# Optimization experiments

Hardware: AMD Instinct MI355X
Metric: run time of the kernel (lower is better)

The kernel has to match this reference:

```python
import jax, jax.numpy as jnp
import numpy as np

MARKER = 50251
BETA_FLOOR = 0.1
LOCAL_SCALE = 0.3
EPS = 1e-6
WINDOW = 256

B, T, D, H, K, V = 4, 1024, 1024, 16, 64, 64
HD = D // H  # SWA head dim


def setup_inputs() -> dict:
    key = jax.random.key(0)
    ks = jax.random.split(key, 16)
    p = lambda i, shape: jax.random.normal(ks[i], shape, jnp.float32) * 0.02
    return dict(
        x=jax.random.normal(ks[0], (B, T, D), jnp.float32),
        initial_state=jnp.zeros((B, H, K, V), jnp.float32),
        W_k=p(1, (D, H * K)),
        W_v=p(2, (D, H * V)),
        W_gdn_o=p(3, (H * V, D)),
        W_beta=p(4, (D, H)), b_beta=jnp.full((H,), -2.0, jnp.float32),
        W_g=p(5, (D, H)), b_g=jnp.full((H,), 2.0, jnp.float32),
        W_lq=p(6, (D, D)), W_lk=p(7, (D, D)), W_lv=p(8, (D, D)),
        W_swa_o=p(9, (D, D)),
        W_ret_o=p(10, (H * V, D)),
        W_gate=p(11, (D, H)), b_gate=jnp.ones((H,), jnp.float32),
        norm_w=jnp.ones((D,), jnp.float32),
        input_ids=jax.random.randint(ks[12], (B, T), 0, 50257, jnp.int32),
    )


def _delta_scan(k, v, beta, g, S0):
    # gated delta rule:  Sd = g_t * S_{t-1};  S_t = Sd + beta_t * k_t (v_t - k_t Sd);  o_t = k_t S_t
    # k:[B,Tm,H,K]  v:[B,Tm,H,V]  beta,g:[B,Tm,H]  S0:[B,H,K,V]
    def step(S, inp):
        kt, vt, bt, gt = inp  # [B,H,K],[B,H,V],[B,H],[B,H]
        Sd = gt[..., None, None] * S
        err = vt - jnp.einsum('bhk,bhkv->bhv', kt, Sd)
        Sn = Sd + bt[..., None, None] * (kt[..., None] * err[:, :, None, :])
        ot = jnp.einsum('bhk,bhkv->bhv', kt, Sn)
        return Sn, ot
    Sf, o = jax.lax.scan(step, S0, (k.transpose(1, 0, 2, 3), v.transpose(1, 0, 2, 3),
                                    beta.transpose(1, 0, 2), g.transpose(1, 0, 2)))
    return o.transpose(1, 0, 2, 3), Sf  # [B,Tm,H,V], [B,H,K,V]


def _forward(x, initial_state, W_k, W_v, W_gdn_o, W_beta, b_beta, W_g, b_g,
             W_lq, W_lk, W_lv, W_swa_o, W_ret_o, W_gate, b_gate, norm_w, input_ids):
    # RMSNorm
    rms = jnp.sqrt(jnp.mean(x * x, axis=-1, keepdims=True) + EPS)
    xn = x / rms * norm_w

    # shared L2-normalized keys and values
    k_shared = (xn @ W_k).reshape(B, T, H, K)
    k_shared = k_shared / jnp.maximum(jnp.linalg.norm(k_shared, axis=-1, keepdims=True), 1e-12)
    v_full = (xn @ W_v).reshape(B, T, H, V)

    # shifted-value GDN inputs (predict next token's value)
    k = k_shared[:, :-1]
    v = v_full[:, 1:]
    beta = jax.nn.sigmoid(xn[:, :-1] @ W_beta + b_beta)  # [B,T-1,H]
    g = jax.nn.sigmoid(xn[:, :-1] @ W_g + b_g)
    marker = (input_ids[:, :-1] == MARKER)[..., None]
    beta = beta * (BETA_FLOOR + (1.0 - BETA_FLOOR) * marker.astype(beta.dtype))

    o, Sf = _delta_scan(k, v, beta, g, initial_state)
    gdn_out = jnp.concatenate([jnp.zeros((B, 1, H, V), o.dtype), o], axis=1)
    gdn_out = gdn_out.reshape(B, T, H * V) @ W_gdn_o  # [B,T,D]

    # sliding-window attention (fallback masked-softmax path)
    q = (xn @ W_lq).reshape(B, T, H, HD).transpose(0, 2, 1, 3)
    kl = (xn @ W_lk).reshape(B, T, H, HD).transpose(0, 2, 1, 3)
    vl = (xn @ W_lv).reshape(B, T, H, HD).transpose(0, 2, 1, 3)
    scale = K ** (-0.5)
    i = jnp.arange(T)[:, None]
    j = jnp.arange(T)[None, :]
    allowed = (j <= i) & (j >= i - WINDOW)  # causal within window
    attn = jnp.einsum('bhqd,bhkd->bhqk', q, kl) * scale
    attn = jnp.where(allowed, attn, -jnp.inf)
    probs = jax.nn.softmax(attn, axis=-1)
    local = jnp.einsum('bhqk,bhkd->bhqd', probs, vl).transpose(0, 2, 1, 3).reshape(B, T, D)
    local_out = LOCAL_SCALE * (local @ W_swa_o)  # eval mode

    # retrieval from final state with shared keys as queries
    retrieved = jnp.einsum('bhkv,bthk->bthv', Sf, k_shared).reshape(B, T, H * V)
    retrieval_out = retrieved @ W_ret_o
    gate = jax.nn.sigmoid(xn @ W_gate + b_gate)  # [B,T,H]
    retrieval_out = jnp.mean(gate, axis=-1, keepdims=True) * retrieval_out

    return x + gdn_out + local_out + retrieval_out


def reference(x, initial_state, W_k, W_v, W_gdn_o, W_beta, b_beta, W_g, b_g,
              W_lq, W_lk, W_lv, W_swa_o, W_ret_o, W_gate, b_gate, norm_w, input_ids):
    return _forward(x, initial_state, W_k, W_v, W_gdn_o, W_beta, b_beta, W_g, b_g,
                    W_lq, W_lk, W_lv, W_swa_o, W_ret_o, W_gate, b_gate, norm_w, input_ids)
```

## Files before the change

kernel.cpp:

```cpp
#include <hip/hip_runtime.h>
#include <hip/hip_bf16.h>

#define BB 4
#define TT 1024
#define DD 1024
#define HH 16
#define KK 64
#define VV 64
#define WIN 256
#define MARKER_ID 50251
#define PSA 5120
#define PSB 3072
#define NPROJ 5248

typedef short bfrag8 __attribute__((ext_vector_type(8)));
typedef float f32x4 __attribute__((ext_vector_type(4)));

static __device__ __forceinline__ unsigned short f2bf(float f) {
  __hip_bfloat16 h = __float2bfloat16(f);
  union { __hip_bfloat16 h; unsigned short u; } cv;
  cv.h = h;
  return cv.u;
}
static __device__ __forceinline__ float bf2f(unsigned short u) {
  union { unsigned int i; float f; } c;
  c.i = ((unsigned int)u) << 16;
  return c.f;
}
static __device__ __forceinline__ void gld_lds16(const unsigned short* g,
                                                 unsigned short* l) {
  __builtin_amdgcn_global_load_lds(
      (const __attribute__((address_space(1))) void*)g,
      (__attribute__((address_space(3))) void*)l, 16, 0, 0);
}

__global__ __launch_bounds__(256) void rmsnorm_kernel(
    const float* __restrict__ x, const float* __restrict__ nw,
    unsigned short* __restrict__ xnb) {
  int row = blockIdx.x;
  int tid = threadIdx.x;
  const float4* xr = (const float4*)(x + (size_t)row * DD);
  float4 v = xr[tid];
  float ss = v.x * v.x + v.y * v.y + v.z * v.z + v.w * v.w;
#pragma unroll
  for (int off = 32; off; off >>= 1) ss += __shfl_xor(ss, off);
  __shared__ float red[4];
  int wid = tid >> 6;
  if ((tid & 63) == 0) red[wid] = ss;
  __syncthreads();
  float tot = red[0] + red[1] + red[2] + red[3];
  float inv = 1.0f / sqrtf(tot * (1.0f / DD) + 1e-6f);
  const float4* wr = (const float4*)nw;
  float4 wv = wr[tid];
  ushort4 o;
  o.x = f2bf(v.x * inv * wv.x);
  o.y = f2bf(v.y * inv * wv.y);
  o.z = f2bf(v.z * inv * wv.z);
  o.w = f2bf(v.w * inv * wv.w);
  *(ushort4*)&xnb[(size_t)row * DD + tid * 4] = o;
}

__global__ __launch_bounds__(256) void convert_wt_kernel(
    const float* W0, const float* W1, const float* W2, const float* W3,
    const float* W4, const float* W5, const float* W6, const float* W7,
    const float* Wb, const float* Wg, const float* Wgt,
    unsigned short* C5, unsigned short* C3) {
  int tid = threadIdx.x;
  if (blockIdx.z == 8) {
    if (blockIdx.x != 0) return;
    int k0 = blockIdx.y * 64;
    for (int e = tid; e < 3 * 16 * 64; e += 256) {
      int w = e >> 10;
      int h = (e >> 6) & 15;
      int kk = e & 63;
      const float* Ws = (w == 0) ? Wb : (w == 1) ? Wg : Wgt;
      C5[(size_t)(5120 + w * 16 + h) * 1024 + k0 + kk] =
          f2bf(Ws[(size_t)(k0 + kk) * 16 + h]);
    }
    for (int e = tid; e < 80 * 64; e += 256) {
      int r = e >> 6, kk = e & 63;
      C5[(size_t)(5168 + r) * 1024 + k0 + kk] = 0;
    }
    return;
  }
  const float* W;
  unsigned short* T;
  int stride;
  float scale = 1.f;
  switch (blockIdx.z) {
    case 0: W = W0; T = C5 + 0 * 1024 * 1024; stride = 1024; break;
    case 1: W = W1; T = C5 + 1 * 1024 * 1024; stride = 1024; break;
    case 2: W = W2; T = C5 + 2 * 1024 * 1024; stride = 1024; break;
    case 3: W = W3; T = C5 + 3 * 1024 * 1024; stride = 1024; break;
    case 4: W = W4; T = C5 + 4 * 1024 * 1024; stride = 1024; break;
    case 5: W = W5; T = C3 + 0; stride = PSB; break;
    case 6: W = W6; T = C3 + 1024; stride = PSB; scale = 0.3f; break;
    default: W = W7; T = C3 + 2048; stride = PSB; break;
  }
  __shared__ float Ts[64][68];
  int n0 = blockIdx.x * 64, k0 = blockIdx.y * 64;
#pragma unroll
  for (int p = 0; p < 4; ++p) {
    int e = p * 256 + tid;
    int k = e >> 4, nq = e & 15;
    float4 w = *(const float4*)&W[(size_t)(k0 + k) * 1024 + n0 + nq * 4];
    Ts[nq * 4 + 0][k] = w.x;
    Ts[nq * 4 + 1][k] = w.y;
    Ts[nq * 4 + 2][k] = w.z;
    Ts[nq * 4 + 3][k] = w.w;
  }
  __syncthreads();
#pragma unroll
  for (int p = 0; p < 4; ++p) {
    int e = p * 256 + tid;
    int n = e >> 4, kq = e & 15;
    float4 v = *(const float4*)&Ts[n][kq * 4];
    ushort4 u;
    u.x = f2bf(v.x * scale);
    u.y = f2bf(v.y * scale);
    u.z = f2bf(v.z * scale);
    u.w = f2bf(v.w * scale);
    *(ushort4*)&T[(size_t)(n0 + n) * stride + k0 + kq * 4] = u;
  }
}

__global__ __launch_bounds__(256) void gemm_out_kernel(
    const unsigned short* __restrict__ A, const unsigned short* __restrict__ BT,
    float* __restrict__ C, const float* __restrict__ addp, int M, int N,
    int K) {
  __shared__ unsigned short As[2][128][32];
  __shared__ unsigned short Bs[2][64][32];
  int flat = blockIdx.y * gridDim.x + blockIdx.x;
  int xcd = flat & 7, local = flat >> 3;
  int m0 = (xcd * 4 + (local & 3)) * 128;
  int n0 = (local >> 2) * 64;
  int tid = threadIdx.x;
  int wave = tid >> 6, lane = tid & 63;
  int wm = wave * 32;
  int r16 = lane & 15, quad = lane >> 4;
  int lrow = lane >> 2, lcol = (lane & 3) * 8;

  f32x4 acc[2][4];
#pragma unroll
  for (int i = 0; i < 2; ++i)
#pragma unroll
    for (int j = 0; j < 4; ++j) acc[i][j] = {0.f, 0.f, 0.f, 0.f};

  auto STAGE = [&](int buf, int kt) {
#pragma unroll
    for (int q = 0; q < 2; ++q) {
      int rb = (wave * 2 + q) * 16;
      gld_lds16(&A[(size_t)(m0 + rb + lrow) * K + kt + lcol], &As[buf][rb][0]);
    }
    {
      int rb = wave * 16;
      gld_lds16(&BT[(size_t)(n0 + rb + lrow) * K + kt + lcol], &Bs[buf][rb][0]);
    }
  };
  auto COMPUTE = [&](int buf) {
    bfrag8 af[2], bq[4];
#pragma unroll
    for (int i = 0; i < 2; ++i)
      af[i] = *(const bfrag8*)&As[buf][wm + i * 16 + r16][quad * 8];
#pragma unroll
    for (int j = 0; j < 4; ++j)
      bq[j] = *(const bfrag8*)&Bs[buf][j * 16 + r16][quad * 8];
#pragma unroll
    for (int i = 0; i < 2; ++i)
#pragma unroll
      for (int j = 0; j < 4; ++j)
        acc[i][j] = __builtin_amdgcn_mfma_f32_16x16x32_bf16(af[i], bq[j],
                                                            acc[i][j], 0, 0, 0);
  };

  STAGE(0, 0);
  STAGE(1, 32);
  asm volatile("s_waitcnt vmcnt(3)" ::: "memory");
  __builtin_amdgcn_s_barrier();
  __builtin_amdgcn_sched_barrier(0);

  int cur = 0;
  for (int kt = 64; kt < K; kt += 32) {
    COMPUTE(cur);
    __builtin_amdgcn_s_barrier();
    STAGE(cur, kt);
    asm volatile("s_waitcnt vmcnt(3)" ::: "memory");
    __builtin_amdgcn_s_barrier();
    __builtin_amdgcn_sched_barrier(0);
    cur ^= 1;
  }
  COMPUTE(cur);
  asm volatile("s_waitcnt vmcnt(0)" ::: "memory");
  __builtin_amdgcn_s_barrier();
  __builtin_amdgcn_sched_barrier(0);
  COMPUTE(cur ^ 1);

#pragma unroll
  for (int i = 0; i < 2; ++i) {
#pragma unroll
    for (int r = 0; r < 4; ++r) {
      int row = m0 + wm + i * 16 + quad * 4 + r;
#pragma unroll
      for (int j = 0; j < 4; ++j) {
        int col = n0 + j * 16 + r16;
        size_t idx = (size_t)row * N + col;
        C[idx] = addp[idx] + acc[i][j][r];
      }
    }
  }
}

__global__ __launch_bounds__(256, 4) void gemm_proj_kernel(
    const unsigned short* __restrict__ A, const unsigned short* __restrict__ BT,
    unsigned short* __restrict__ PALL, float* __restrict__ SPRJ) {
  const int K = 1024;
  __shared__ unsigned short As[2][128][32];
  __shared__ unsigned short Bs[2][128][32];
  int flat = blockIdx.y * gridDim.x + blockIdx.x;
  int xcd = flat & 7, local = flat >> 3;
  int mi = local & 3, ni = local >> 2;
  int m0 = (xcd * 4 + mi) * 128;
  int n0 = ni * 128;
  int tid = threadIdx.x;
  int wave = tid >> 6, lane = tid & 63;
  int wm = (wave & 1) * 64, wn = (wave >> 1) * 64;
  int r16 = lane & 15, quad = lane >> 4;
  int lrow = lane >> 2, lcol = (lane & 3) * 8;

  f32x4 acc[4][4];
#pragma unroll
  for (int i = 0; i < 4; ++i)
#pragma unroll
    for (int j = 0; j < 4; ++j) acc[i][j] = {0.f, 0.f, 0.f, 0.f};

#pragma unroll
  for (int q = 0; q < 2; ++q) {
    int rb = (wave * 2 + q) * 16;
    gld_lds16(&A[(size_t)(m0 + rb + lrow) * K + lcol], &As[0][rb][0]);
    gld_lds16(&BT[(size_t)(n0 + rb + lrow) * K + lcol], &Bs[0][rb][0]);
  }
  __syncthreads();

  int cur = 0;
  for (int kt = 32; kt < K; kt += 32) {
#pragma unroll
    for (int q = 0; q < 2; ++q) {
      int rb = (wave * 2 + q) * 16;
      gld_lds16(&A[(size_t)(m0 + rb + lrow) * K + kt + lcol],
                &As[cur ^ 1][rb][0]);
      gld_lds16(&BT[(size_t)(n0 + rb + lrow) * K + kt + lcol],
                &Bs[cur ^ 1][rb][0]);
    }
    bfrag8 af[4], bq[4];
#pragma unroll
    for (int i = 0; i < 4; ++i) {
      af[i] = *(const bfrag8*)&As[cur][wm + i * 16 + r16][quad * 8];
      bq[i] = *(const bfrag8*)&Bs[cur][wn + i * 16 + r16][quad * 8];
    }
#pragma unroll
    for (int i = 0; i < 4; ++i)
#pragma unroll
      for (int j = 0; j < 4; ++j)
        acc[i][j] = __builtin_amdgcn_mfma_f32_16x16x32_bf16(af[i], bq[j],
                                                            acc[i][j], 0, 0, 0);
    __syncthreads();
    cur ^= 1;
  }
  {
    bfrag8 af[4], bq[4];
#pragma unroll
    for (int i = 0; i < 4; ++i) {
      af[i] = *(const bfrag8*)&As[cur][wm + i * 16 + r16][quad * 8];
      bq[i] = *(const bfrag8*)&Bs[cur][wn + i * 16 + r16][quad * 8];
    }
#pragma unroll
    for (int i = 0; i < 4; ++i)
#pragma unroll
      for (int j = 0; j < 4; ++j)
        acc[i][j] = __builtin_amdgcn_mfma_f32_16x16x32_bf16(af[i], bq[j],
                                                            acc[i][j], 0, 0, 0);
  }
  bool gates = (n0 >= 5120);
#pragma unroll
  for (int i = 0; i < 4; ++i) {
#pragma unroll
    for (int r = 0; r < 4; ++r) {
      int row = m0 + wm + i * 16 + quad * 4 + r;
#pragma unroll
      for (int j = 0; j < 4; ++j) {
        int col = n0 + wn + j * 16 + r16;
        if (!gates)
          PALL[(size_t)row * PSA + col] = f2bf(acc[i][j][r]);
        else
          SPRJ[(size_t)row * 128 + col - 5120] = acc[i][j][r];
      }
    }
  }
}

__global__ __launch_bounds__(256) void gates_kernel(
    const float* __restrict__ SPRJ, const float* __restrict__ bb,
    const float* __restrict__ bg, const float* __restrict__ bgt,
    const int* __restrict__ ids, float* __restrict__ beta,
    float* __restrict__ g, float* __restrict__ mg) {
  int row = blockIdx.x * 4 + (threadIdx.x >> 6);
  int lane = threadIdx.x & 63;
  if (lane < 48) {
    int h = lane & 15;
    float v = SPRJ[(size_t)row * 128 + lane];
    float bias = (lane < 16) ? bb[h] : (lane < 32) ? bg[h] : bgt[h];
    float s = 1.f / (1.f + __expf(-(v + bias)));
    if (lane < 16) {
      float mk = (ids[row] == MARKER_ID) ? 1.f : 0.1f;
      beta[(size_t)row * 16 + h] = s * mk;
    } else if (lane < 32) {
      g[(size_t)row * 16 + h] = s;
    } else {
      float sum = s;
#pragma unroll
      for (int off = 1; off < 16; off <<= 1) sum += __shfl_xor(sum, off);
      if (lane == 32) mg[row] = sum * (1.f / 16.f);
    }
  }
}

__global__ __launch_bounds__(256) void knorm_kernel(
    unsigned short* __restrict__ pall) {
  int w = blockIdx.x * 4 + (threadIdx.x >> 6);
  int lane = threadIdx.x & 63;
  size_t addr = (size_t)(w >> 4) * PSA + (w & 15) * 64 + lane;
  float v = bf2f(pall[addr]);
  float ss = v * v;
#pragma unroll
  for (int off = 32; off; off >>= 1) ss += __shfl_xor(ss, off);
  float n = sqrtf(ss);
  n = fmaxf(n, 1e-12f);
  pall[addr] = f2bf(v / n);
}

__global__ __launch_bounds__(256) void attn_mfma_kernel(
    const unsigned short* __restrict__ PALL, unsigned short* __restrict__ ACAT) {
  __shared__ unsigned short Qs[64][72];
  __shared__ unsigned short Ks[64][72];
  __shared__ unsigned short Vt[64][72];
  __shared__ unsigned short Ps[64][72];
  int qb = blockIdx.x * 64;
  int bh = blockIdx.y;
  int h = bh & 15, b = bh >> 4;
  int tid = threadIdx.x, lane = tid & 63, wave = tid >> 6;
  int r16 = lane & 15, quad = lane >> 4;
  int m0w = wave * 16;
  const unsigned short* Qg = PALL + (size_t)b * TT * PSA + 2048 + h * 64;
  const unsigned short* Kg = Qg + 1024;
  const unsigned short* Vg = Qg + 2048;
  int sr = tid >> 2, sq = tid & 3;
  {
    *(uint4*)&Qs[sr][sq * 16] =
        *(const uint4*)&Qg[(size_t)(qb + sr) * PSA + sq * 16];
    *(uint4*)&Qs[sr][sq * 16 + 8] =
        *(const uint4*)&Qg[(size_t)(qb + sr) * PSA + sq * 16 + 8];
  }
  float m[4], l[4];
  f32x4 o[4];
#pragma unroll
  for (int r = 0; r < 4; ++r) {
    m[r] = -1e30f;
    l[r] = 0.f;
    o[r] = {0.f, 0.f, 0.f, 0.f};
  }
  int kt0 = qb - (int)WIN;
  if (kt0 < 0) kt0 = 0;

  for (int kt = kt0; kt <= qb; kt += 64) {
    __syncthreads();
    {
      *(uint4*)&Ks[sr][sq * 16] =
          *(const uint4*)&Kg[(size_t)(kt + sr) * PSA + sq * 16];
      *(uint4*)&Ks[sr][sq * 16 + 8] =
          *(const uint4*)&Kg[(size_t)(kt + sr) * PSA + sq * 16 + 8];
      union { uint4 u4[2]; unsigned short s[16]; } vv;
      vv.u4[0] = *(const uint4*)&Vg[(size_t)(kt + sr) * PSA + sq * 16];
      vv.u4[1] = *(const uint4*)&Vg[(size_t)(kt + sr) * PSA + sq * 16 + 8];
#pragma unroll
      for (int i = 0; i < 16; ++i) Vt[sq * 16 + i][sr] = vv.s[i];
    }
    __syncthreads();
    bfrag8 af0 = *(const bfrag8*)&Qs[m0w + r16][quad * 8];
    bfrag8 af1 = *(const bfrag8*)&Qs[m0w + r16][quad * 8 + 32];
    f32x4 s[4];
#pragma unroll
    for (int j = 0; j < 4; ++j) s[j] = {0.f, 0.f, 0.f, 0.f};
#pragma unroll
    for (int j = 0; j < 4; ++j) {
      bfrag8 b0 = *(const bfrag8*)&Ks[j * 16 + r16][quad * 8];
      bfrag8 b1 = *(const bfrag8*)&Ks[j * 16 + r16][quad * 8 + 32];
      s[j] = __builtin_amdgcn_mfma_f32_16x16x32_bf16(af0, b0, s[j], 0, 0, 0);
      s[j] = __builtin_amdgcn_mfma_f32_16x16x32_bf16(af1, b1, s[j], 0, 0, 0);
    }
    bool oldest = (kt == qb - (int)WIN);
    bool newest = (kt == qb);
#pragma unroll
    for (int r = 0; r < 4; ++r) {
      int il = m0w + quad * 4 + r;
      float sv[4];
#pragma unroll
      for (int j = 0; j < 4; ++j) {
        int jl = j * 16 + r16;
        float v = s[j][r] * 0.125f;
        if (oldest && jl < il) v = -1e30f;
        if (newest && jl > il) v = -1e30f;
        sv[j] = v;
      }
      float mx = fmaxf(fmaxf(sv[0], sv[1]), fmaxf(sv[2], sv[3]));
#pragma unroll
      for (int off = 1; off < 16; off <<= 1) mx = fmaxf(mx, __shfl_xor(mx, off));
      float mn = fmaxf(m[r], mx);
      float al = __expf(m[r] - mn);
      m[r] = mn;
      float rs = 0.f;
#pragma unroll
      for (int j = 0; j < 4; ++j) {
        float p = __expf(sv[j] - mn);
        rs += p;
        Ps[il][j * 16 + r16] = f2bf(p);
      }
#pragma unroll
      for (int off = 1; off < 16; off <<= 1) rs += __shfl_xor(rs, off);
      l[r] = l[r] * al + rs;
#pragma unroll
      for (int j = 0; j < 4; ++j) o[j][r] *= al;
    }
    bfrag8 pa0 = *(const bfrag8*)&Ps[m0w + r16][quad * 8];
    bfrag8 pa1 = *(const bfrag8*)&Ps[m0w + r16][quad * 8 + 32];
#pragma unroll
    for (int j = 0; j < 4; ++j) {
      bfrag8 v0 = *(const bfrag8*)&Vt[j * 16 + r16][quad * 8];
      bfrag8 v1 = *(const bfrag8*)&Vt[j * 16 + r16][quad * 8 + 32];
      o[j] = __builtin_amdgcn_mfma_f32_16x16x32_bf16(pa0, v0, o[j], 0, 0, 0);
      o[j] = __builtin_amdgcn_mfma_f32_16x16x32_bf16(pa1, v1, o[j], 0, 0, 0);
    }
  }
#pragma unroll
  for (int r = 0; r < 4; ++r) {
    int row = m0w + quad * 4 + r;
    float inv = 1.f / l[r];
#pragma unroll
    for (int j = 0; j < 4; ++j) {
      ACAT[((size_t)(b * TT + qb + row)) * PSB + 1024 + h * 64 + j * 16 + r16] =
          f2bf(o[j][r] * inv);
    }
  }
}

__global__ __launch_bounds__(256) void scan_phaseA(
    const unsigned short* __restrict__ PALL, const float* __restrict__ beta,
    const float* __restrict__ g, unsigned short* __restrict__ UFg,
    unsigned short* __restrict__ Zg, unsigned short* __restrict__ Pg,
    unsigned short* __restrict__ Qg, float* __restrict__ Ag) {
  __shared__ unsigned short Kc[64][72];
  __shared__ unsigned short KTb[64][72];
  __shared__ float Vc[64][68];
  __shared__ float Msv[64][68];
  __shared__ unsigned short UFT[64][72];
  __shared__ unsigned short ZTl[64][72];
  __shared__ float aArr[64], iaArr[64], bArr[64], baArr[64], sKT[64];
  __shared__ float aCs;

  int c = blockIdx.x, bh = blockIdx.y;
  int b = bh >> 4, h = bh & 15;
  int tc = c * 64;
  int tid = threadIdx.x, lane = tid & 63, wave = tid >> 6;
  int r16 = lane & 15, quad = lane >> 4;
  int m0w = wave * 16;
  size_t bhc = (size_t)bh * 16 + c;

  const unsigned short* kbase = PALL + ((size_t)b * TT) * PSA + h * 64;
  const unsigned short* vbase = kbase + 1024;
  const float* bbase = beta + ((size_t)b * TT) * HH + h;
  const float* gbase = g + ((size_t)b * TT) * HH + h;

  if (tid < 64) {
    int ts = tc + tid;
    bool pad = (ts > 1022);
    float gv = pad ? 1.f : gbase[(size_t)ts * HH];
    float bv = pad ? 0.f : bbase[(size_t)ts * HH];
    float p = gv;
#pragma unroll
    for (int o = 1; o < 64; o <<= 1) {
      float t = __shfl_up(p, o);
      if (lane >= o) p *= t;
    }
    aArr[tid] = p;
    iaArr[tid] = 1.f / p;
    bArr[tid] = bv;
    baArr[tid] = bv * p;
    float aC = __shfl(p, 63);
    sKT[tid] = aC / p;
    if (tid == 0) aCs = aC;
    Ag[bhc * 64 + tid] = p;
  }
  __syncthreads();
  {
    int r = tid >> 2, q = tid & 3;
    int ts = tc + r;
    float skt = sKT[r];
    union { uint4 u4[2]; unsigned short s[16]; } kv;
    kv.u4[0] = *(const uint4*)&kbase[(size_t)ts * PSA + q * 16];
    kv.u4[1] = *(const uint4*)&kbase[(size_t)ts * PSA + q * 16 + 8];
    *(uint4*)&Kc[r][q * 16] = kv.u4[0];
    *(uint4*)&Kc[r][q * 16 + 8] = kv.u4[1];
#pragma unroll
    for (int i = 0; i < 16; ++i)
      KTb[q * 16 + i][r] = f2bf(bf2f(kv.s[i]) * skt);
    if (ts <= 1022) {
      union { uint4 u4[2]; unsigned short s[16]; } vv;
      vv.u4[0] = *(const uint4*)&vbase[(size_t)(ts + 1) * PSA + q * 16];
      vv.u4[1] = *(const uint4*)&vbase[(size_t)(ts + 1) * PSA + q * 16 + 8];
#pragma unroll
      for (int i = 0; i < 16; ++i) Vc[r][q * 16 + i] = bf2f(vv.s[i]);
    } else {
#pragma unroll
      for (int i = 0; i < 16; ++i) Vc[r][q * 16 + i] = 0.f;
    }
  }
  __syncthreads();
  {
    bfrag8 af0 = *(const bfrag8*)&Kc[m0w + r16][quad * 8];
    bfrag8 af1 = *(const bfrag8*)&Kc[m0w + r16][quad * 8 + 32];
    f32x4 acc1[4];
#pragma unroll
    for (int j = 0; j < 4; ++j) acc1[j] = {0.f, 0.f, 0.f, 0.f};
#pragma unroll
    for (int j = 0; j < 4; ++j) {
      bfrag8 k0 = *(const bfrag8*)&Kc[j * 16 + r16][quad * 8];
      bfrag8 k1 = *(const bfrag8*)&Kc[j * 16 + r16][quad * 8 + 32];
      acc1[j] = __builtin_amdgcn_mfma_f32_16x16x32_bf16(af0, k0, acc1[j], 0, 0, 0);
      acc1[j] = __builtin_amdgcn_mfma_f32_16x16x32_bf16(af1, k1, acc1[j], 0, 0, 0);
    }
#pragma unroll
    for (int j = 0; j < 4; ++j) {
#pragma unroll
      for (int r = 0; r < 4; ++r) {
        int row = m0w + quad * 4 + r;
        int col = j * 16 + r16;
        Msv[row][col] =
            (col < row) ? bArr[row] * aArr[row] * iaArr[col] * acc1[j][r] : 0.f;
      }
    }
  }
  __syncthreads();
  if (wave < 2) {
    float u[64];
    if (wave == 0) {
#pragma unroll
      for (int t = 0; t < 64; ++t) u[t] = bArr[t] * Vc[t][lane];
    } else {
#pragma unroll
      for (int t = 0; t < 64; ++t) u[t] = baArr[t] * bf2f(Kc[t][lane]);
    }
#pragma unroll
    for (int t = 1; t < 64; ++t) {
      float a0 = 0.f, a1 = 0.f, a2 = 0.f, a3 = 0.f;
#pragma unroll
      for (int s4 = 0; s4 * 4 < t; ++s4) {
        float4 mr = *(const float4*)&Msv[t][s4 * 4];
        a0 = fmaf(mr.x, u[s4 * 4 + 0], a0);
        a1 = fmaf(mr.y, u[s4 * 4 + 1], a1);
        a2 = fmaf(mr.z, u[s4 * 4 + 2], a2);
        a3 = fmaf(mr.w, u[s4 * 4 + 3], a3);
      }
      u[t] -= (a0 + a1) + (a2 + a3);
    }
    unsigned short* Tls = (wave == 0) ? &UFT[lane][0] : &ZTl[lane][0];
#pragma unroll
    for (int t2 = 0; t2 < 32; ++t2) {
      unsigned int pk = (unsigned int)f2bf(u[2 * t2]) |
                        ((unsigned int)f2bf(u[2 * t2 + 1]) << 16);
      *(unsigned int*)&Tls[2 * t2] = pk;
    }
    unsigned short* Gn = (wave == 0) ? UFg : Zg;
#pragma unroll
    for (int t = 0; t < 64; ++t) {
      Gn[(bhc * 64 + t) * 64 + lane] = f2bf(u[t]);
    }
  }
  __syncthreads();
  {
    bfrag8 af0 = *(const bfrag8*)&KTb[m0w + r16][quad * 8];
    bfrag8 af1 = *(const bfrag8*)&KTb[m0w + r16][quad * 8 + 32];
    f32x4 accp[4], accq[4];
#pragma unroll
    for (int j = 0; j < 4; ++j) {
      accp[j] = {0.f, 0.f, 0.f, 0.f};
      accq[j] = {0.f, 0.f, 0.f, 0.f};
    }
#pragma unroll
    for (int j = 0; j < 4; ++j) {
      bfrag8 z0 = *(const bfrag8*)&ZTl[j * 16 + r16][quad * 8];
      bfrag8 z1 = *(const bfrag8*)&ZTl[j * 16 + r16][quad * 8 + 32];
      accp[j] = __builtin_amdgcn_mfma_f32_16x16x32_bf16(af0, z0, accp[j], 0, 0, 0);
      accp[j] = __builtin_amdgcn_mfma_f32_16x16x32_bf16(af1, z1, accp[j], 0, 0, 0);
      bfrag8 u0 = *(const bfrag8*)&UFT[j * 16 + r16][quad * 8];
      bfrag8 u1 = *(const bfrag8*)&UFT[j * 16 + r16][quad * 8 + 32];
      accq[j] = __builtin_amdgcn_mfma_f32_16x16x32_bf16(af0, u0, accq[j], 0, 0, 0);
      accq[j] = __builtin_amdgcn_mfma_f32_16x16x32_bf16(af1, u1, accq[j], 0, 0, 0);
    }
    float aC = aCs;
#pragma unroll
    for (int j = 0; j < 4; ++j) {
#pragma unroll
      for (int r = 0; r < 4; ++r) {
        int row = m0w + quad * 4 + r;
        int col = j * 16 + r16;
        float pv = ((row == col) ? aC : 0.f) - accp[j][r];
        Pg[bhc * 4096 + (size_t)row * 64 + col] = f2bf(pv);
        Qg[bhc * 4096 + (size_t)row * 64 + col] = f2bf(accq[j][r]);
      }
    }
  }
}

__global__ __launch_bounds__(256) void scan_phaseB(
    const float* __restrict__ S0, const unsigned short* __restrict__ Pg,
    const unsigned short* __restrict__ Qg, unsigned short* __restrict__ SinTg,
    float* __restrict__ Sf, unsigned short* __restrict__ ACAT) {
  __shared__ unsigned short STb[64][72];
  __shared__ unsigned short Pl[64][72];
  int bh = blockIdx.x;
  int b = bh >> 4, h = bh & 15;
  int tid = threadIdx.x, lane = tid & 63, wave = tid >> 6;
  int r16 = lane & 15, quad = lane >> 4;
  int m0w = wave * 16;
  int rr = tid >> 2, qq = tid & 3;
  {
    const float* s0p = S0 + (size_t)bh * 4096;
#pragma unroll
    for (int i = 0; i < 4; ++i) {
      float4 sv = *(const float4*)&s0p[rr * 64 + qq * 16 + i * 4];
      STb[qq * 16 + i * 4 + 0][rr] = f2bf(sv.x);
      STb[qq * 16 + i * 4 + 1][rr] = f2bf(sv.y);
      STb[qq * 16 + i * 4 + 2][rr] = f2bf(sv.z);
      STb[qq * 16 + i * 4 + 3][rr] = f2bf(sv.w);
    }
    if (tid < 64) ACAT[((size_t)b * TT) * PSB + h * 64 + tid] = 0;
  }
  for (int c = 0; c < 16; ++c) {
    size_t bhc = (size_t)bh * 16 + c;
    __syncthreads();
    {
      uint4 s0v = *(const uint4*)&STb[rr][qq * 16];
      uint4 s1v = *(const uint4*)&STb[rr][qq * 16 + 8];
      *(uint4*)&SinTg[bhc * 4096 + (size_t)rr * 64 + qq * 16] = s0v;
      *(uint4*)&SinTg[bhc * 4096 + (size_t)rr * 64 + qq * 16 + 8] = s1v;
      uint4 p0 = *(const uint4*)&Pg[bhc * 4096 + (size_t)rr * 64 + qq * 16];
      uint4 p1 = *(const uint4*)&Pg[bhc * 4096 + (size_t)rr * 64 + qq * 16 + 8];
      *(uint4*)&Pl[rr][qq * 16] = p0;
      *(uint4*)&Pl[rr][qq * 16 + 8] = p1;
    }
    __syncthreads();
    f32x4 acc[4];
#pragma unroll
    for (int j = 0; j < 4; ++j) acc[j] = {0.f, 0.f, 0.f, 0.f};
    {
      bfrag8 af0 = *(const bfrag8*)&Pl[m0w + r16][quad * 8];
      bfrag8 af1 = *(const bfrag8*)&Pl[m0w + r16][quad * 8 + 32];
#pragma unroll
      for (int j = 0; j < 4; ++j) {
        bfrag8 s0v = *(const bfrag8*)&STb[j * 16 + r16][quad * 8];
        bfrag8 s1v = *(const bfrag8*)&STb[j * 16 + r16][quad * 8 + 32];
        acc[j] = __builtin_amdgcn_mfma_f32_16x16x32_bf16(af0, s0v, acc[j], 0, 0, 0);
        acc[j] = __builtin_amdgcn_mfma_f32_16x16x32_bf16(af1, s1v, acc[j], 0, 0, 0);
      }
    }
    float snew[4][4];
#pragma unroll
    for (int j = 0; j < 4; ++j) {
#pragma unroll
      for (int r = 0; r < 4; ++r) {
        int row = m0w + quad * 4 + r;
        int col = j * 16 + r16;
        snew[j][r] = acc[j][r] + bf2f(Qg[bhc * 4096 + (size_t)row * 64 + col]);
      }
    }
    __syncthreads();
#pragma unroll
    for (int j = 0; j < 4; ++j) {
#pragma unroll
      for (int r = 0; r < 4; ++r) {
        int row = m0w + quad * 4 + r;
        int col = j * 16 + r16;
        STb[col][row] = f2bf(snew[j][r]);
        if (c == 15) Sf[(size_t)bh * 4096 + (size_t)row * 64 + col] = snew[j][r];
      }
    }
  }
}

__global__ __launch_bounds__(256) void scan_phaseC(
    const unsigned short* __restrict__ PALL,
    const unsigned short* __restrict__ UFg,
    const unsigned short* __restrict__ Zg,
    const unsigned short* __restrict__ SinTg, const float* __restrict__ Ag,
    unsigned short* __restrict__ ACAT) {
  __shared__ unsigned short Kc[64][72];
  __shared__ unsigned short SvT[64][72];
  __shared__ unsigned short Zl[64][72];
  __shared__ unsigned short Ufl[64][72];
  __shared__ unsigned short Wl[64][72];
  __shared__ unsigned short UTl[64][72];
  __shared__ float aA[64], iaA[64];

  int c = blockIdx.x, bh = blockIdx.y;
  int b = bh >> 4, h = bh & 15;
  int tc = c * 64;
  int tid = threadIdx.x, lane = tid & 63, wave = tid >> 6;
  int r16 = lane & 15, quad = lane >> 4;
  int m0w = wave * 16;
  size_t bhc = (size_t)bh * 16 + c;
  const unsigned short* kbase = PALL + ((size_t)b * TT) * PSA + h * 64;

  if (tid < 64) {
    float av = Ag[bhc * 64 + tid];
    aA[tid] = av;
    iaA[tid] = 1.f / av;
  }
  {
    int r = tid >> 2, q = tid & 3;
    int ts = tc + r;
    *(uint4*)&Kc[r][q * 16] = *(const uint4*)&kbase[(size_t)ts * PSA + q * 16];
    *(uint4*)&Kc[r][q * 16 + 8] =
        *(const uint4*)&kbase[(size_t)ts * PSA + q * 16 + 8];
    uint4 sv0 = *(const uint4*)&SinTg[bhc * 4096 + (size_t)r * 64 + q * 16];
    uint4 sv1 = *(const uint4*)&SinTg[bhc * 4096 + (size_t)r * 64 + q * 16 + 8];
    *(uint4*)&SvT[r][q * 16] = sv0;
    *(uint4*)&SvT[r][q * 16 + 8] = sv1;
    uint4 zv0 = *(const uint4*)&Zg[(bhc * 64 + r) * 64 + q * 16];
    uint4 zv1 = *(const uint4*)&Zg[(bhc * 64 + r) * 64 + q * 16 + 8];
    *(uint4*)&Zl[r][q * 16] = zv0;
    *(uint4*)&Zl[r][q * 16 + 8] = zv1;
    uint4 uv0 = *(const uint4*)&UFg[(bhc * 64 + r) * 64 + q * 16];
    uint4 uv1 = *(const uint4*)&UFg[(bhc * 64 + r) * 64 + q * 16 + 8];
    *(uint4*)&Ufl[r][q * 16] = uv0;
    *(uint4*)&Ufl[r][q * 16 + 8] = uv1;
  }
  __syncthreads();
  float op[4][4];
  {
    bfrag8 af0 = *(const bfrag8*)&Kc[m0w + r16][quad * 8];
    bfrag8 af1 = *(const bfrag8*)&Kc[m0w + r16][quad * 8 + 32];
    bfrag8 zf0 = *(const bfrag8*)&Zl[m0w + r16][quad * 8];
    bfrag8 zf1 = *(const bfrag8*)&Zl[m0w + r16][quad * 8 + 32];
    f32x4 acc1[4], acc2[4], acc3[4];
#pragma unroll
    for (int j = 0; j < 4; ++j) {
      acc1[j] = {0.f, 0.f, 0.f, 0.f};
      acc2[j] = {0.f, 0.f, 0.f, 0.f};
      acc3[j] = {0.f, 0.f, 0.f, 0.f};
    }
#pragma unroll
    for (int j = 0; j < 4; ++j) {
      bfrag8 k0 = *(const bfrag8*)&Kc[j * 16 + r16][quad * 8];
      bfrag8 k1 = *(const bfrag8*)&Kc[j * 16 + r16][quad * 8 + 32];
      acc1[j] = __builtin_amdgcn_mfma_f32_16x16x32_bf16(af0, k0, acc1[j], 0, 0, 0);
      acc1[j] = __builtin_amdgcn_mfma_f32_16x16x32_bf16(af1, k1, acc1[j], 0, 0, 0);
      bfrag8 s0 = *(const bfrag8*)&SvT[j * 16 + r16][quad * 8];
      bfrag8 s1 = *(const bfrag8*)&SvT[j * 16 + r16][quad * 8 + 32];
      acc3[j] = __builtin_amdgcn_mfma_f32_16x16x32_bf16(af0, s0, acc3[j], 0, 0, 0);
      acc3[j] = __builtin_amdgcn_mfma_f32_16x16x32_bf16(af1, s1, acc3[j], 0, 0, 0);
      acc2[j] = __builtin_amdgcn_mfma_f32_16x16x32_bf16(zf0, s0, acc2[j], 0, 0, 0);
      acc2[j] = __builtin_amdgcn_mfma_f32_16x16x32_bf16(zf1, s1, acc2[j], 0, 0, 0);
    }
#pragma unroll
    for (int j = 0; j < 4; ++j) {
#pragma unroll
      for (int r = 0; r < 4; ++r) {
        int row = m0w + quad * 4 + r;
        int col = j * 16 + r16;
        Wl[row][col] = (col <= row) ? f2bf(aA[row] * iaA[col] * acc1[j][r])
                                    : (unsigned short)0;
        float uval = bf2f(Ufl[row][col]) - acc2[j][r];
        UTl[col][row] = f2bf(uval);
        op[j][r] = aA[row] * acc3[j][r];
      }
    }
  }
  __syncthreads();
  {
    bfrag8 wf0 = *(const bfrag8*)&Wl[m0w + r16][quad * 8];
    bfrag8 wf1 = *(const bfrag8*)&Wl[m0w + r16][quad * 8 + 32];
    f32x4 acc4[4];
#pragma unroll
    for (int j = 0; j < 4; ++j) acc4[j] = {0.f, 0.f, 0.f, 0.f};
#pragma unroll
    for (int j = 0; j < 4; ++j) {
      bfrag8 u0 = *(const bfrag8*)&UTl[j * 16 + r16][quad * 8];
      bfrag8 u1 = *(const bfrag8*)&UTl[j * 16 + r16][quad * 8 + 32];
      acc4[j] = __builtin_amdgcn_mfma_f32_16x16x32_bf16(wf0, u0, acc4[j], 0, 0, 0);
      acc4[j] = __builtin_amdgcn_mfma_f32_16x16x32_bf16(wf1, u1, acc4[j], 0, 0, 0);
    }
#pragma unroll
    for (int j = 0; j < 4; ++j) {
#pragma unroll
      for (int r = 0; r < 4; ++r) {
        int row = m0w + quad * 4 + r;
        int col = j * 16 + r16;
        int ts = tc + row;
        if (ts < 1023) {
          ACAT[((size_t)b * TT + ts + 1) * PSB + h * 64 + col] =
              f2bf(op[j][r] + acc4[j][r]);
        }
      }
    }
  }
}

__global__ __launch_bounds__(256) void retrieve_kernel(
    const unsigned short* __restrict__ PALL, const float* __restrict__ Sf,
    const float* __restrict__ mg, unsigned short* __restrict__ ACAT) {
  __shared__ float Sfs[64][64];
  int tc = blockIdx.x * 64;
  int bh = blockIdx.y;
  int b = bh >> 4, h = bh & 15;
  int tid = threadIdx.x, lane = tid & 63, wave = tid >> 6;
  const float* sfp = Sf + (size_t)bh * 4096;
#pragma unroll
  for (int i = 0; i < 4; ++i) {
    int e = tid + i * 256;
    ((float4*)&Sfs[0][0])[e] = ((const float4*)sfp)[e];
  }
  __syncthreads();
  const unsigned short* kb = PALL + ((size_t)b * TT) * PSA + h * 64;
#pragma unroll 2
  for (int ti = 0; ti < 16; ++ti) {
    int t = tc + wave * 16 + ti;
    size_t bt = (size_t)b * TT + t;
    float kl = bf2f(kb[(size_t)t * PSA + lane]);
    float a0 = 0.f, a1 = 0.f, a2 = 0.f, a3 = 0.f;
#pragma unroll
    for (int k = 0; k < 64; k += 4) {
      a0 = fmaf(__shfl(kl, k + 0), Sfs[k + 0][lane], a0);
      a1 = fmaf(__shfl(kl, k + 1), Sfs[k + 1][lane], a1);
      a2 = fmaf(__shfl(kl, k + 2), Sfs[k + 2][lane], a2);
      a3 = fmaf(__shfl(kl, k + 3), Sfs[k + 3][lane], a3);
    }
    float acc = (a0 + a1) + (a2 + a3);
    ACAT[bt * PSB + 2048 + h * 64 + lane] = f2bf(acc * mg[bt]);
  }
}

extern "C" void kernel_launch(void* const* d_in, const int* in_sizes, int n_in,
                              void* d_out, int out_size, void* d_ws,
                              size_t ws_size, hipStream_t stream) {
  (void)in_sizes; (void)n_in; (void)out_size; (void)ws_size;
  const float* x       = (const float*)d_in[0];
  const float* S0      = (const float*)d_in[1];
  const float* W_k     = (const float*)d_in[2];
  const float* W_v     = (const float*)d_in[3];
  const float* W_gdn_o = (const float*)d_in[4];
  const float* W_beta  = (const float*)d_in[5];
  const float* b_beta  = (const float*)d_in[6];
  const float* W_g     = (const float*)d_in[7];
  const float* b_g     = (const float*)d_in[8];
  const float* W_lq    = (const float*)d_in[9];
  const float* W_lk    = (const float*)d_in[10];
  const float* W_lv    = (const float*)d_in[11];
  const float* W_swa_o = (const float*)d_in[12];
  const float* W_ret_o = (const float*)d_in[13];
  const float* W_gate  = (const float*)d_in[14];
  const float* b_gate  = (const float*)d_in[15];
  const float* norm_w  = (const float*)d_in[16];
  const int*   ids     = (const int*)d_in[17];
  float* out = (float*)d_out;

  char* ws = (char*)d_ws;
  size_t off = 0;
  auto allocf = [&](size_t n) {
    float* p = (float*)(ws + off);
    off += n * sizeof(float);
    return p;
  };
  auto allocu = [&](size_t n) {
    unsigned short* p = (unsigned short*)(ws + off);
    off += n * sizeof(unsigned short);
    return p;
  };
  const int M = BB * TT;
  unsigned short* XNb    = allocu((size_t)M * DD);
  unsigned short* PALL   = allocu((size_t)M * PSA);
  unsigned short* ACAT   = allocu((size_t)M * PSB);
  float*          SPRJ   = allocf((size_t)M * 128);
  unsigned short* WTcat5 = allocu((size_t)NPROJ * 1024);
  unsigned short* WTcat3 = allocu((size_t)1024 * PSB);
  float* BETA = allocf((size_t)M * HH);
  float* Gg   = allocf((size_t)M * HH);
  float* MG   = allocf((size_t)M);
  float* SF   = allocf((size_t)BB * HH * KK * VV);
  const size_t CH = (size_t)BB * HH * 16 * 64 * 64;
  unsigned short* UFg   = allocu(CH);
  unsigned short* Zg    = allocu(CH);
  unsigned short* Pg    = allocu(CH);
  unsigned short* Qg    = allocu(CH);
  unsigned short* SinTg = allocu(CH);
  float* Ag = allocf((size_t)BB * HH * 16 * 64);

  rmsnorm_kernel<<<M, 256, 0, stream>>>(x, norm_w, XNb);

  convert_wt_kernel<<<dim3(16, 16, 9), 256, 0, stream>>>(
      W_k, W_v, W_lq, W_lk, W_lv, W_gdn_o, W_swa_o, W_ret_o, W_beta, W_g,
      W_gate, WTcat5, WTcat3);

  gemm_proj_kernel<<<dim3(41, 32), 256, 0, stream>>>(XNb, WTcat5, PALL, SPRJ);

  knorm_kernel<<<(M * HH) / 4, 256, 0, stream>>>(PALL);
  gates_kernel<<<M / 4, 256, 0, stream>>>(SPRJ, b_beta, b_g, b_gate, ids, BETA,
                                          Gg, MG);

  scan_phaseA<<<dim3(16, BB * HH), 256, 0, stream>>>(PALL, BETA, Gg, UFg, Zg,
                                                     Pg, Qg, Ag);
  scan_phaseB<<<BB * HH, 256, 0, stream>>>(S0, Pg, Qg, SinTg, SF, ACAT);
  scan_phaseC<<<dim3(16, BB * HH), 256, 0, stream>>>(PALL, UFg, Zg, SinTg, Ag,
                                                     ACAT);

  attn_mfma_kernel<<<dim3(TT / 64, BB * HH), 256, 0, stream>>>(PALL, ACAT);

  retrieve_kernel<<<dim3(TT / 64, BB * HH), 256, 0, stream>>>(PALL, SF, MG,
                                                              ACAT);

  gemm_out_kernel<<<dim3(16, 32), 256, 0, stream>>>(ACAT, WTcat3, out, x, M, DD,
                                                    3072);
}
```

Before: 382.5 us.

## Merge small kernels into combined launches and prefetch K/V tiles in SWA attention

Folds rmsnorm and weight conversion into one prep kernel, knorm and gates into one kernel, and scan phase C and retrieval into one kernel that picks its role from the block index and shares an LDS union. This cuts the launch count and lets independent small jobs run side by side. Separately, the sliding-window attention kernel now loads the next K/V tile into registers while computing on the current one, and loads the Q fragments once instead of every iteration. The costs are higher register pressure in attention and a larger shared-memory footprint in the merged scan/retrieve kernel.

```diff
diff --git a/kernel.cpp b/kernel.cpp
--- a/kernel.cpp
+++ b/kernel.cpp
@@ -34,17 +34,15 @@
       (__attribute__((address_space(3))) void*)l, 16, 0, 0);
 }
 
-__global__ __launch_bounds__(256) void rmsnorm_kernel(
-    const float* __restrict__ x, const float* __restrict__ nw,
-    unsigned short* __restrict__ xnb) {
-  int row = blockIdx.x;
+static __device__ __forceinline__ void rmsnorm_body(
+    int row, const float* __restrict__ x, const float* __restrict__ nw,
+    unsigned short* __restrict__ xnb, float* red) {
   int tid = threadIdx.x;
   const float4* xr = (const float4*)(x + (size_t)row * DD);
   float4 v = xr[tid];
   float ss = v.x * v.x + v.y * v.y + v.z * v.z + v.w * v.w;
 #pragma unroll
   for (int off = 32; off; off >>= 1) ss += __shfl_xor(ss, off);
-  __shared__ float red[4];
   int wid = tid >> 6;
   if ((tid & 63) == 0) red[wid] = ss;
   __syncthreads();
@@ -60,15 +58,15 @@
   *(ushort4*)&xnb[(size_t)row * DD + tid * 4] = o;
 }
 
-__global__ __launch_bounds__(256) void convert_wt_kernel(
-    const float* W0, const float* W1, const float* W2, const float* W3,
-    const float* W4, const float* W5, const float* W6, const float* W7,
-    const float* Wb, const float* Wg, const float* Wgt,
-    unsigned short* C5, unsigned short* C3) {
+static __device__ __forceinline__ void convert_body(
+    int xb, int yb, int zb, const float* W0, const float* W1, const float* W2,
+    const float* W3, const float* W4, const float* W5, const float* W6,
+    const float* W7, const float* Wb, const float* Wg, const float* Wgt,
+    unsigned short* C5, unsigned short* C3, float (*Ts)[68]) {
   int tid = threadIdx.x;
-  if (blockIdx.z == 8) {
-    if (blockIdx.x != 0) return;
-    int k0 = blockIdx.y * 64;
+  if (zb == 8) {
+    if (xb != 0) return;
+    int k0 = yb * 64;
     for (int e = tid; e < 3 * 16 * 64; e += 256) {
       int w = e >> 10;
       int h = (e >> 6) & 15;
@@ -87,7 +85,7 @@
   unsigned short* T;
   int stride;
   float scale = 1.f;
-  switch (blockIdx.z) {
+  switch (zb) {
     case 0: W = W0; T = C5 + 0 * 1024 * 1024; stride = 1024; break;
     case 1: W = W1; T = C5 + 1 * 1024 * 1024; stride = 1024; break;
     case 2: W = W2; T = C5 + 2 * 1024 * 1024; stride = 1024; break;
@@ -97,8 +95,7 @@
     case 6: W = W6; T = C3 + 1024; stride = PSB; scale = 0.3f; break;
     default: W = W7; T = C3 + 2048; stride = PSB; break;
   }
-  __shared__ float Ts[64][68];
-  int n0 = blockIdx.x * 64, k0 = blockIdx.y * 64;
+  int n0 = xb * 64, k0 = yb * 64;
 #pragma unroll
   for (int p = 0; p < 4; ++p) {
     int e = p * 256 + tid;
@@ -121,6 +118,23 @@
     u.z = f2bf(v.z * scale);
     u.w = f2bf(v.w * scale);
     *(ushort4*)&T[(size_t)(n0 + n) * stride + k0 + kq * 4] = u;
+  }
+}
+
+__global__ __launch_bounds__(256) void prep_kernel(
+    const float* __restrict__ x, const float* __restrict__ nw,
+    unsigned short* __restrict__ xnb, const float* W0, const float* W1,
+    const float* W2, const float* W3, const float* W4, const float* W5,
+    const float* W6, const float* W7, const float* Wb, const float* Wg,
+    const float* Wgt, unsigned short* C5, unsigned short* C3) {
+  __shared__ __align__(16) float Ts[64][68];
+  int f = blockIdx.x;
+  if (f < 4096) {
+    rmsnorm_body(f, x, nw, xnb, &Ts[0][0]);
+  } else {
+    int c = f - 4096;
+    convert_body(c & 15, (c >> 4) & 15, c >> 8, W0, W1, W2, W3, W4, W5, W6, W7,
+                 Wb, Wg, Wgt, C5, C3, Ts);
   }
 }
 
@@ -298,44 +312,44 @@
   }
 }
 
-__global__ __launch_bounds__(256) void gates_kernel(
-    const float* __restrict__ SPRJ, const float* __restrict__ bb,
-    const float* __restrict__ bg, const float* __restrict__ bgt,
-    const int* __restrict__ ids, float* __restrict__ beta,
-    float* __restrict__ g, float* __restrict__ mg) {
-  int row = blockIdx.x * 4 + (threadIdx.x >> 6);
-  int lane = threadIdx.x & 63;
-  if (lane < 48) {
-    int h = lane & 15;
-    float v = SPRJ[(size_t)row * 128 + lane];
-    float bias = (lane < 16) ? bb[h] : (lane < 32) ? bg[h] : bgt[h];
-    float s = 1.f / (1.f + __expf(-(v + bias)));
-    if (lane < 16) {
-      float mk = (ids[row] == MARKER_ID) ? 1.f : 0.1f;
-      beta[(size_t)row * 16 + h] = s * mk;
-    } else if (lane < 32) {
-      g[(size_t)row * 16 + h] = s;
-    } else {
-      float sum = s;
-#pragma unroll
-      for (int off = 1; off < 16; off <<= 1) sum += __shfl_xor(sum, off);
-      if (lane == 32) mg[row] = sum * (1.f / 16.f);
-    }
-  }
-}
-
-__global__ __launch_bounds__(256) void knorm_kernel(
-    unsigned short* __restrict__ pall) {
-  int w = blockIdx.x * 4 + (threadIdx.x >> 6);
-  int lane = threadIdx.x & 63;
-  size_t addr = (size_t)(w >> 4) * PSA + (w & 15) * 64 + lane;
-  float v = bf2f(pall[addr]);
-  float ss = v * v;
-#pragma unroll
-  for (int off = 32; off; off >>= 1) ss += __shfl_xor(ss, off);
-  float n = sqrtf(ss);
-  n = fmaxf(n, 1e-12f);
-  pall[addr] = f2bf(v / n);
+__global__ __launch_bounds__(256) void ng_kernel(
+    unsigned short* __restrict__ pall, const float* __restrict__ SPRJ,
+    const float* __restrict__ bb, const float* __restrict__ bg,
+    const float* __restrict__ bgt, const int* __restrict__ ids,
+    float* __restrict__ beta, float* __restrict__ g, float* __restrict__ mg) {
+  int f = blockIdx.x;
+  if (f < 16384) {
+    int w = f * 4 + (threadIdx.x >> 6);
+    int lane = threadIdx.x & 63;
+    size_t addr = (size_t)(w >> 4) * PSA + (w & 15) * 64 + lane;
+    float v = bf2f(pall[addr]);
+    float ss = v * v;
+#pragma unroll
+    for (int off = 32; off; off >>= 1) ss += __shfl_xor(ss, off);
+    float n = sqrtf(ss);
+    n = fmaxf(n, 1e-12f);
+    pall[addr] = f2bf(v / n);
+  } else {
+    int row = (f - 16384) * 4 + (threadIdx.x >> 6);
+    int lane = threadIdx.x & 63;
+    if (lane < 48) {
+      int h = lane & 15;
+      float v = SPRJ[(size_t)row * 128 + lane];
+      float bias = (lane < 16) ? bb[h] : (lane < 32) ? bg[h] : bgt[h];
+      float s = 1.f / (1.f + __expf(-(v + bias)));
+      if (lane < 16) {
+        float mk = (ids[row] == MARKER_ID) ? 1.f : 0.1f;
+        beta[(size_t)row * 16 + h] = s * mk;
+      } else if (lane < 32) {
+        g[(size_t)row * 16 + h] = s;
+      } else {
+        float sum = s;
+#pragma unroll
+        for (int off = 1; off < 16; off <<= 1) sum += __shfl_xor(sum, off);
+        if (lane == 32) mg[row] = sum * (1.f / 16.f);
+      }
+    }
+  }
 }
 
 __global__ __launch_bounds__(256) void attn_mfma_kernel(
@@ -354,12 +368,32 @@
   const unsigned short* Kg = Qg + 1024;
   const unsigned short* Vg = Qg + 2048;
   int sr = tid >> 2, sq = tid & 3;
+  int kt0 = qb - (int)WIN;
+  if (kt0 < 0) kt0 = 0;
+
+  uint4 kr0, kr1;
+  union { uint4 u4[2]; unsigned short s[16]; } vr;
   {
     *(uint4*)&Qs[sr][sq * 16] =
         *(const uint4*)&Qg[(size_t)(qb + sr) * PSA + sq * 16];
     *(uint4*)&Qs[sr][sq * 16 + 8] =
         *(const uint4*)&Qg[(size_t)(qb + sr) * PSA + sq * 16 + 8];
-  }
+    kr0 = *(const uint4*)&Kg[(size_t)(kt0 + sr) * PSA + sq * 16];
+    kr1 = *(const uint4*)&Kg[(size_t)(kt0 + sr) * PSA + sq * 16 + 8];
+    vr.u4[0] = *(const uint4*)&Vg[(size_t)(kt0 + sr) * PSA + sq * 16];
+    vr.u4[1] = *(const uint4*)&Vg[(size_t)(kt0 + sr) * PSA + sq * 16 + 8];
+  }
+  __syncthreads();
+  bfrag8 af0 = *(const bfrag8*)&Qs[m0w + r16][quad * 8];
+  bfrag8 af1 = *(const bfrag8*)&Qs[m0w + r16][quad * 8 + 32];
+  {
+    *(uint4*)&Ks[sr][sq * 16] = kr0;
+    *(uint4*)&Ks[sr][sq * 16 + 8] = kr1;
+#pragma unroll
+    for (int i = 0; i < 16; ++i) Vt[sq * 16 + i][sr] = vr.s[i];
+  }
+  __syncthreads();
+
   float m[4], l[4];
   f32x4 o[4];
 #pragma unroll
@@ -368,25 +402,15 @@
     l[r] = 0.f;
     o[r] = {0.f, 0.f, 0.f, 0.f};
   }
-  int kt0 = qb - (int)WIN;
-  if (kt0 < 0) kt0 = 0;
 
   for (int kt = kt0; kt <= qb; kt += 64) {
-    __syncthreads();
-    {
-      *(uint4*)&Ks[sr][sq * 16] =
-          *(const uint4*)&Kg[(size_t)(kt + sr) * PSA + sq * 16];
-      *(uint4*)&Ks[sr][sq * 16 + 8] =
-          *(const uint4*)&Kg[(size_t)(kt + sr) * PSA + sq * 16 + 8];
-      union { uint4 u4[2]; unsigned short s[16]; } vv;
-      vv.u4[0] = *(const uint4*)&Vg[(size_t)(kt + sr) * PSA + sq * 16];
-      vv.u4[1] = *(const uint4*)&Vg[(size_t)(kt + sr) * PSA + sq * 16 + 8];
-#pragma unroll
-      for (int i = 0; i < 16; ++i) Vt[sq * 16 + i][sr] = vv.s[i];
-    }
-    __syncthreads();
-    bfrag8 af0 = *(const bfrag8*)&Qs[m0w + r16][quad * 8];
-    bfrag8 af1 = *(const bfrag8*)&Qs[m0w + r16][quad * 8 + 32];
+    bool more = (kt + 64 <= qb);
+    if (more) {
+      kr0 = *(const uint4*)&Kg[(size_t)(kt + 64 + sr) * PSA + sq * 16];
+      kr1 = *(const uint4*)&Kg[(size_t)(kt + 64 + sr) * PSA + sq * 16 + 8];
+      vr.u4[0] = *(const uint4*)&Vg[(size_t)(kt + 64 + sr) * PSA + sq * 16];
+      vr.u4[1] = *(const uint4*)&Vg[(size_t)(kt + 64 + sr) * PSA + sq * 16 + 8];
+    }
     f32x4 s[4];
 #pragma unroll
     for (int j = 0; j < 4; ++j) s[j] = {0.f, 0.f, 0.f, 0.f};
@@ -438,6 +462,14 @@
       bfrag8 v1 = *(const bfrag8*)&Vt[j * 16 + r16][quad * 8 + 32];
       o[j] = __builtin_amdgcn_mfma_f32_16x16x32_bf16(pa0, v0, o[j], 0, 0, 0);
       o[j] = __builtin_amdgcn_mfma_f32_16x16x32_bf16(pa1, v1, o[j], 0, 0, 0);
+    }
+    if (more) {
+      __syncthreads();
+      *(uint4*)&Ks[sr][sq * 16] = kr0;
+      *(uint4*)&Ks[sr][sq * 16 + 8] = kr1;
+#pragma unroll
+      for (int i = 0; i < 16; ++i) Vt[sq * 16 + i][sr] = vr.s[i];
+      __syncthreads();
     }
   }
 #pragma unroll
@@ -696,21 +728,30 @@
   }
 }
 
-__global__ __launch_bounds__(256) void scan_phaseC(
-    const unsigned short* __restrict__ PALL,
+union Sm3 {
+  struct {
+    unsigned short Kc[64][72], SvT[64][72], Zl[64][72], Ufl[64][72],
+        Wl[64][72], UTl[64][72];
+    float aA[64], iaA[64];
+  } sc;
+  struct { float Sfs[64][64]; } rt;
+};
+
+static __device__ void scanC_body(
+    int c, int bh, const unsigned short* __restrict__ PALL,
     const unsigned short* __restrict__ UFg,
     const unsigned short* __restrict__ Zg,
     const unsigned short* __restrict__ SinTg, const float* __restrict__ Ag,
-    unsigned short* __restrict__ ACAT) {
-  __shared__ unsigned short Kc[64][72];
-  __shared__ unsigned short SvT[64][72];
-  __shared__ unsigned short Zl[64][72];
-  __shared__ unsigned short Ufl[64][72];
-  __shared__ unsigned short Wl[64][72];
-  __shared__ unsigned short UTl[64][72];
-  __shared__ float aA[64], iaA[64];
-
-  int c = blockIdx.x, bh = blockIdx.y;
+    unsigned short* __restrict__ ACAT, Sm3& sm) {
+  auto& Kc = sm.sc.Kc;
+  auto& SvT = sm.sc.SvT;
+  auto& Zl = sm.sc.Zl;
+  auto& Ufl = sm.sc.Ufl;
+  auto& Wl = sm.sc.Wl;
+  auto& UTl = sm.sc.UTl;
+  auto& aA = sm.sc.aA;
+  auto& iaA = sm.sc.iaA;
+
   int b = bh >> 4, h = bh & 15;
   int tc = c * 64;
   int tid = threadIdx.x, lane = tid & 63, wave = tid >> 6;
@@ -814,12 +855,12 @@
   }
 }
 
-__global__ __launch_bounds__(256) void retrieve_kernel(
-    const unsigned short* __restrict__ PALL, const float* __restrict__ Sf,
-    const float* __restrict__ mg, unsigned short* __restrict__ ACAT) {
-  __shared__ float Sfs[64][64];
-  int tc = blockIdx.x * 64;
-  int bh = blockIdx.y;
+static __device__ void retrieve_body(
+    int cx, int bh, const unsigned short* __restrict__ PALL,
+    const float* __restrict__ Sf, const float* __restrict__ mg,
+    unsigned short* __restrict__ ACAT, Sm3& sm) {
+  auto& Sfs = sm.rt.Sfs;
+  int tc = cx * 64;
   int b = bh >> 4, h = bh & 15;
   int tid = threadIdx.x, lane = tid & 63, wave = tid >> 6;
   const float* sfp = Sf + (size_t)bh * 4096;
@@ -846,6 +887,23 @@
     float acc = (a0 + a1) + (a2 + a3);
     ACAT[bt * PSB + 2048 + h * 64 + lane] = f2bf(acc * mg[bt]);
   }
+}
+
+__global__ __launch_bounds__(256) void scanC_retr_kernel(
+    const unsigned short* __restrict__ PALL,
+    const unsigned short* __restrict__ UFg,
+    const unsigned short* __restrict__ Zg,
+    const unsigned short* __restrict__ SinTg, const float* __restrict__ Ag,
+    const float* __restrict__ Sf, const float* __restrict__ mg,
+    unsigned short* __restrict__ ACAT) {
+  __shared__ Sm3 sm;
+  int bx = blockIdx.x;
+  int sel = bx & 1, idx = bx >> 1;
+  int cx = idx & 15, bh = idx >> 4;
+  if (sel == 0)
+    scanC_body(cx, bh, PALL, UFg, Zg, SinTg, Ag, ACAT, sm);
+  else
+    retrieve_body(cx, bh, PALL, Sf, mg, ACAT, sm);
 }
 
 extern "C" void kernel_launch(void* const* d_in, const int* in_sizes, int n_in,
@@ -857,8 +915,8 @@
   const float* W_k     = (const float*)d_in[2];
   const float* W_v     = (const float*)d_in[3];
   const float* W_gdn_o = (const float*)d_in[4];
+  const float* b_beta  = (const float*)d_in[6];
   const float* W_beta  = (const float*)d_in[5];
-  const float* b_beta  = (const float*)d_in[6];
   const float* W_g     = (const float*)d_in[7];
   const float* b_g     = (const float*)d_in[8];
   const float* W_lq    = (const float*)d_in[9];
@@ -903,28 +961,23 @@
   unsigned short* SinTg = allocu(CH);
   float* Ag = allocf((size_t)BB * HH * 16 * 64);
 
-  rmsnorm_kernel<<<M, 256, 0, stream>>>(x, norm_w, XNb);
-
-  convert_wt_kernel<<<dim3(16, 16, 9), 256, 0, stream>>>(
-      W_k, W_v, W_lq, W_lk, W_lv, W_gdn_o, W_swa_o, W_ret_o, W_beta, W_g,
-      W_gate, WTcat5, WTcat3);
+  prep_kernel<<<6400, 256, 0, stream>>>(x, norm_w, XNb, W_k, W_v, W_lq, W_lk,
+                                        W_lv, W_gdn_o, W_swa_o, W_ret_o,
+                                        W_beta, W_g, W_gate, WTcat5, WTcat3);
 
   gemm_proj_kernel<<<dim3(41, 32), 256, 0, stream>>>(XNb, WTcat5, PALL, SPRJ);
 
-  knorm_kernel<<<(M * HH) / 4, 256, 0, stream>>>(PALL);
-  gates_kernel<<<M / 4, 256, 0, stream>>>(SPRJ, b_beta, b_g, b_gate, ids, BETA,
-                                          Gg, MG);
+  ng_kernel<<<17408, 256, 0, stream>>>(PALL, SPRJ, b_beta, b_g, b_gate, ids,
+                                       BETA, Gg, MG);
 
   scan_phaseA<<<dim3(16, BB * HH), 256, 0, stream>>>(PALL, BETA, Gg, UFg, Zg,
                                                      Pg, Qg, Ag);
   scan_phaseB<<<BB * HH, 256, 0, stream>>>(S0, Pg, Qg, SinTg, SF, ACAT);
-  scan_phaseC<<<dim3(16, BB * HH), 256, 0, stream>>>(PALL, UFg, Zg, SinTg, Ag,
-                                                     ACAT);
 
   attn_mfma_kernel<<<dim3(TT / 64, BB * HH), 256, 0, stream>>>(PALL, ACAT);
 
-  retrieve_kernel<<<dim3(TT / 64, BB * HH), 256, 0, stream>>>(PALL, SF, MG,
-                                                              ACAT);
+  scanC_retr_kernel<<<2048, 256, 0, stream>>>(PALL, UFg, Zg, SinTg, Ag, SF, MG,
+                                              ACAT);
 
   gemm_out_kernel<<<dim3(16, 32), 256, 0, stream>>>(ACAT, WTcat3, out, x, M, DD,
                                                     3072);
```

Measured after the change: 423.7 us. 10.8% more time.
